# Kernel tuning notes

Measured on AMD Instinct MI355X. Metric: run time of the kernel, lower is better.

Reference implementation:

```python
import jax, jax.numpy as jnp
import numpy as np

EPS = 0.05  # blend weight of K_Rectify smoothing


def k_rectify(x_nbc, distance, idx, eps=EPS):
    """Distance-weighted neighbor smoothing.
    x_nbc: (N, B, C); distance, idx: (B, N, K). Returns (N, B, C)."""
    x_bnc = jnp.transpose(x_nbc, (1, 0, 2))                       # (B,N,C)
    B = x_bnc.shape[0]
    neigh = x_bnc[jnp.arange(B)[:, None, None], idx]              # (B,N,K,C) gather
    w = jax.nn.softmax(-distance, axis=-1)                        # closer -> larger weight
    smoothed = jnp.einsum('bnk,bnkc->bnc', w, neigh)              # (B,N,C)
    y = (1.0 - eps) * x_bnc + eps * smoothed
    return jnp.transpose(y, (1, 0, 2))


def monarch_linear(x, w1, w2, bias):
    """Monarch block-diagonal butterfly multiply on the last dim.
    w1: (k,q,p), w2: (l,s,r) with k*p == n, l*r == k*q."""
    shp = x.shape
    k, q, p = w1.shape
    l, s, r = w2.shape
    xb = x.reshape(-1, k, p)
    o1 = jnp.einsum('kqp,bkp->bkq', w1, xb)                       # (B*, k, q)
    o1 = o1.reshape(-1, r, l).transpose(0, 2, 1)                  # 'b (r l) -> b l r'
    o2 = jnp.einsum('lsr,blr->bls', w2, o1)                       # (B*, l, s)
    out = o2.transpose(0, 2, 1).reshape(-1, s * l) + bias         # 'b l s -> b (s l)'
    return out.reshape(*shp[:-1], s * l)


def setup_inputs() -> dict:
    key = jax.random.key(0)
    B, N, C, K, nblocks = 8, 8192, 256, 8, 8
    blk = C // nblocks
    ks = jax.random.split(key, 6)
    x = jax.random.normal(ks[0], (B, N, C), dtype=jnp.float32)
    distance = jax.random.uniform(ks[1], (B, N, K), dtype=jnp.float32)
    idx = jax.random.randint(ks[2], (B, N, K), 0, N)
    rf = jax.random.normal(ks[3], (B, N, C), dtype=jnp.float32)
    scale = 1.0 / np.sqrt(blk)
    w1 = jax.random.normal(ks[4], (nblocks, blk, blk), dtype=jnp.float32) * scale
    w2 = jax.random.normal(ks[5], (nblocks, blk, blk), dtype=jnp.float32) * scale
    bias = jnp.zeros((C,), dtype=jnp.float32)
    return {"x": x, "distance": distance, "idx": idx, "rf": rf,
            "w1": w1, "w2": w2, "bias": bias}


def reference(x, distance, idx, rf, w1, w2, bias):
    # _prepare_in: (B,N,C) -> (N,B,C)
    xs = jnp.transpose(x, (1, 0, 2))
    s1 = k_rectify(xs, distance, idx)            # smooth_in
    t = monarch_linear(s1, w1, w2, bias)         # Monarch block-diag matmul
    s2 = k_rectify(t, distance, idx)             # smooth_out
    return jnp.transpose(s2, (1, 0, 2)) + rf     # _out_transform residual
```

## Files before the change

### kernel.cpp

```cpp
#include <hip/hip_runtime.h>

#define NPTS 8192
#define CH   256
#define KNB  8
#define NROWS 65536
#define ROWS_PER_BLK 32
#define ROWS_PER_IT  4
#define FT_STRIDE 36

#define NBLK_CONV 8192
#define NBLK_S1   (NROWS / ROWS_PER_BLK)
#define NBLK_S2   (NROWS / 16)

typedef unsigned short ushort_t;
typedef float  f32x4  __attribute__((ext_vector_type(4)));

__device__ __forceinline__ int xcd_swz(int h, int cpx) {
    return (h & 7) * cpx + (h >> 3);
}

__device__ __forceinline__ ushort_t f32_to_bf16(float f) {
    unsigned int b = __float_as_uint(f);
    b += 0x7FFFu + ((b >> 16) & 1u);
    return (ushort_t)(b >> 16);
}
__device__ __forceinline__ float bf16_to_f32(ushort_t u) {
    return __uint_as_float(((unsigned int)u) << 16);
}
__device__ __forceinline__ unsigned int pack_bf16(float lo, float hi) {
    return (unsigned int)f32_to_bf16(lo) | ((unsigned int)f32_to_bf16(hi) << 16);
}

__global__ __launch_bounds__(256) void pm_conv(
    const f32x4* __restrict__ x, uint4* __restrict__ xb)
{
    const int l = xcd_swz(blockIdx.x, NBLK_CONV / 8);
    const size_t i = (size_t)l * 256 + threadIdx.x;
    const f32x4 a = __builtin_nontemporal_load(&x[2 * i]);
    const f32x4 c = __builtin_nontemporal_load(&x[2 * i + 1]);
    uint4 o;
    o.x = pack_bf16(a.x, a.y);
    o.y = pack_bf16(a.z, a.w);
    o.z = pack_bf16(c.x, c.y);
    o.w = pack_bf16(c.z, c.w);
    xb[i] = o;
}

__global__ __launch_bounds__(256) void pm_stage1(
    const ushort_t* __restrict__ xb, const float* __restrict__ dist,
    const int* __restrict__ idx, const float* __restrict__ w1,
    const float* __restrict__ w2, const float* __restrict__ bias,
    ushort_t* __restrict__ t)
{
    const int c = threadIdx.x;

    __shared__ float s1[ROWS_PER_IT][CH];
    __shared__ float fT[ROWS_PER_IT][8 * FT_STRIDE];

    float4 w1r[8], w2r[8];
    {
        const float4* w1p = (const float4*)(w1 + c * 32);
        const float4* w2p = (const float4*)(w2 + ((c & 7) * 32 + (c >> 3)) * 32);
#pragma unroll
        for (int i = 0; i < 8; ++i) { w1r[i] = w1p[i]; w2r[i] = w2p[i]; }
    }
    const float bb = bias[c];
    const int l2   = c & 7;
    const int kb   = c >> 5;
    const int ftw  = l2 * FT_STRIDE + (c >> 3);

    const int rr   = __builtin_amdgcn_readfirstlane(threadIdx.x >> 6);
    const int lane = threadIdx.x & 63;

    const int lb       = xcd_swz(blockIdx.x, NBLK_S1 / 8);
    const int row_base = lb * ROWS_PER_BLK;
    const int b = row_base >> 13;
    const ushort4* x4 = (const ushort4*)(xb + (size_t)b * NPTS * CH);

    for (int it = 0; it < ROWS_PER_BLK / ROWS_PER_IT; ++it) {
        const int row  = row_base + it * ROWS_PER_IT + rr;
        const int rloc = row & (NPTS - 1);

        float d[KNB]; int nb[KNB];
#pragma unroll
        for (int k = 0; k < KNB; ++k) {
            d[k]  = dist[(size_t)row * KNB + k];
            nb[k] = idx[(size_t)row * KNB + k];
        }

        const ushort4 c0 = x4[(size_t)rloc * 64 + lane];
        ushort4 g[KNB];
#pragma unroll
        for (int k = 0; k < KNB; ++k) g[k] = x4[(size_t)nb[k] * 64 + lane];

        float mn = d[0];
#pragma unroll
        for (int k = 1; k < KNB; ++k) mn = fminf(mn, d[k]);
        float e[KNB]; float sum = 0.f;
#pragma unroll
        for (int k = 0; k < KNB; ++k) { e[k] = __expf(mn - d[k]); sum += e[k]; }
        const float inv = 0.05f / sum;

        float4 acc;
        acc.x = 0.95f * bf16_to_f32(c0.x);
        acc.y = 0.95f * bf16_to_f32(c0.y);
        acc.z = 0.95f * bf16_to_f32(c0.z);
        acc.w = 0.95f * bf16_to_f32(c0.w);
#pragma unroll
        for (int k = 0; k < KNB; ++k) {
            const float w = e[k] * inv;
            acc.x += w * bf16_to_f32(g[k].x);
            acc.y += w * bf16_to_f32(g[k].y);
            acc.z += w * bf16_to_f32(g[k].z);
            acc.w += w * bf16_to_f32(g[k].w);
        }
        ((float4*)&s1[rr][0])[lane] = acc;
        __syncthreads();

#pragma unroll
        for (int r2 = 0; r2 < ROWS_PER_IT; ++r2) {
            const float4* sb = (const float4*)(&s1[r2][kb * 32]);
            float a = 0.f;
#pragma unroll
            for (int p4 = 0; p4 < 8; ++p4) {
                const float4 s = sb[p4];
                a += w1r[p4].x * s.x + w1r[p4].y * s.y
                   + w1r[p4].z * s.z + w1r[p4].w * s.w;
            }
            fT[r2][ftw] = a;
        }
        __syncthreads();

#pragma unroll
        for (int r2 = 0; r2 < ROWS_PER_IT; ++r2) {
            const float4* fp = (const float4*)(&fT[r2][l2 * FT_STRIDE]);
            float a = bb;
#pragma unroll
            for (int r4 = 0; r4 < 8; ++r4) {
                const float4 f = fp[r4];
                a += w2r[r4].x * f.x + w2r[r4].y * f.y
                   + w2r[r4].z * f.z + w2r[r4].w * f.w;
            }
            __builtin_nontemporal_store(
                f32_to_bf16(a),
                &t[(size_t)(row_base + it * ROWS_PER_IT + r2) * CH + c]);
        }
        __syncthreads();
    }
}

__global__ __launch_bounds__(256) void pm_stage2(
    const ushort_t* __restrict__ t, const float* __restrict__ dist,
    const int* __restrict__ idx, const float* __restrict__ rf,
    float* __restrict__ out)
{
    const int w     = __builtin_amdgcn_readfirstlane(threadIdx.x >> 6);
    const int lane  = threadIdx.x & 63;
    const int lb    = xcd_swz(blockIdx.x, NBLK_S2 / 8);
    const int wrow0 = lb * 16 + w * 4;
    const int b     = wrow0 >> 13;
    const ushort4* tb = (const ushort4*)(t + (size_t)b * NPTS * CH);

    int   nb[4][KNB];
    float d [4][KNB];
#pragma unroll
    for (int r = 0; r < 4; ++r)
#pragma unroll
        for (int k = 0; k < KNB; ++k) {
            nb[r][k] = idx[(size_t)(wrow0 + r) * KNB + k];
            d [r][k] = dist[(size_t)(wrow0 + r) * KNB + k];
        }

    ushort4 c0[4], g[4][KNB];
    f32x4   rv[4];
#pragma unroll
    for (int r = 0; r < 4; ++r) {
        const int rloc = (wrow0 + r) & (NPTS - 1);
        c0[r] = tb[(size_t)rloc * 64 + lane];
        rv[r] = __builtin_nontemporal_load(
                    &((const f32x4*)rf)[(size_t)(wrow0 + r) * 64 + lane]);
#pragma unroll
        for (int k = 0; k < KNB; ++k) g[r][k] = tb[(size_t)nb[r][k] * 64 + lane];
    }

#pragma unroll
    for (int r = 0; r < 4; ++r) {
        float mn = d[r][0];
#pragma unroll
        for (int k = 1; k < KNB; ++k) mn = fminf(mn, d[r][k]);
        float e[KNB]; float sum = 0.f;
#pragma unroll
        for (int k = 0; k < KNB; ++k) { e[k] = __expf(mn - d[r][k]); sum += e[k]; }
        const float inv = 0.05f / sum;

        f32x4 acc;
        acc.x = 0.95f * bf16_to_f32(c0[r].x) + rv[r].x;
        acc.y = 0.95f * bf16_to_f32(c0[r].y) + rv[r].y;
        acc.z = 0.95f * bf16_to_f32(c0[r].z) + rv[r].z;
        acc.w = 0.95f * bf16_to_f32(c0[r].w) + rv[r].w;
#pragma unroll
        for (int k = 0; k < KNB; ++k) {
            const float wk = e[k] * inv;
            acc.x += wk * bf16_to_f32(g[r][k].x);
            acc.y += wk * bf16_to_f32(g[r][k].y);
            acc.z += wk * bf16_to_f32(g[r][k].z);
            acc.w += wk * bf16_to_f32(g[r][k].w);
        }
        __builtin_nontemporal_store(
            acc, &((f32x4*)out)[(size_t)(wrow0 + r) * 64 + lane]);
    }
}

extern "C" void kernel_launch(void* const* d_in, const int* in_sizes, int n_in,
                              void* d_out, int out_size, void* d_ws, size_t ws_size,
                              hipStream_t stream) {
    const float* x    = (const float*)d_in[0];
    const float* dist = (const float*)d_in[1];
    const int*   idx  = (const int*)d_in[2];
    const float* rf   = (const float*)d_in[3];
    const float* w1   = (const float*)d_in[4];
    const float* w2   = (const float*)d_in[5];
    const float* bias = (const float*)d_in[6];
    float* out = (float*)d_out;

    ushort_t* t  = (ushort_t*)d_ws;
    ushort_t* xb = (ushort_t*)((char*)d_ws + (size_t)NROWS * CH * 2);

    pm_conv  <<<NBLK_CONV, 256, 0, stream>>>((const f32x4*)x, (uint4*)xb);
    pm_stage1<<<NBLK_S1,   256, 0, stream>>>(xb, dist, idx, w1, w2, bias, t);
    pm_stage2<<<NBLK_S2,   256, 0, stream>>>(t, dist, idx, rf, out);
}
```

Baseline: 270.1 us.

## Software-pipeline neighbor gathers in stage1 and scalarize index loads

Stage1 now prefetches the next iteration's distances, indices and neighbor gathers while the Monarch matmul for the current rows runs, and drops the trailing barrier per iteration. Barriers become a manual lgkmcnt wait plus s_barrier, so outstanding global loads are not drained at each sync. Index and distance loads are vectorized and neighbor indices are made wave-uniform via readfirstlane, so gather addresses become scalar. Launch bounds ask for 4 blocks per CU, which may limit registers, and the extra prefetched values raise register pressure.

```diff
diff --git a/kernel.cpp b/kernel.cpp
--- a/kernel.cpp
+++ b/kernel.cpp
@@ -6,6 +6,7 @@
 #define NROWS 65536
 #define ROWS_PER_BLK 32
 #define ROWS_PER_IT  4
+#define NIT (ROWS_PER_BLK / ROWS_PER_IT)
 #define FT_STRIDE 36
 
 #define NBLK_CONV 8192
@@ -14,6 +15,11 @@
 
 typedef unsigned short ushort_t;
 typedef float  f32x4  __attribute__((ext_vector_type(4)));
+
+#define BARRIER_LDS() do { \
+    asm volatile("s_waitcnt lgkmcnt(0)" ::: "memory"); \
+    __builtin_amdgcn_s_barrier(); \
+} while (0)
 
 __device__ __forceinline__ int xcd_swz(int h, int cpx) {
     return (h & 7) * cpx + (h >> 3);
@@ -46,7 +52,7 @@
     xb[i] = o;
 }
 
-__global__ __launch_bounds__(256) void pm_stage1(
+__global__ __launch_bounds__(256, 4) void pm_stage1(
     const ushort_t* __restrict__ xb, const float* __restrict__ dist,
     const int* __restrict__ idx, const float* __restrict__ w1,
     const float* __restrict__ w2, const float* __restrict__ bias,
@@ -75,30 +81,51 @@
     const int lb       = xcd_swz(blockIdx.x, NBLK_S1 / 8);
     const int row_base = lb * ROWS_PER_BLK;
     const int b = row_base >> 13;
-    const ushort4* x4 = (const ushort4*)(xb + (size_t)b * NPTS * CH);
-
-    for (int it = 0; it < ROWS_PER_BLK / ROWS_PER_IT; ++it) {
-        const int row  = row_base + it * ROWS_PER_IT + rr;
-        const int rloc = row & (NPTS - 1);
-
-        float d[KNB]; int nb[KNB];
-#pragma unroll
-        for (int k = 0; k < KNB; ++k) {
-            d[k]  = dist[(size_t)row * KNB + k];
-            nb[k] = idx[(size_t)row * KNB + k];
-        }
-
-        const ushort4 c0 = x4[(size_t)rloc * 64 + lane];
-        ushort4 g[KNB];
-#pragma unroll
-        for (int k = 0; k < KNB; ++k) g[k] = x4[(size_t)nb[k] * 64 + lane];
-
-        float mn = d[0];
-#pragma unroll
-        for (int k = 1; k < KNB; ++k) mn = fminf(mn, d[k]);
+    const char* xbase  = (const char*)(xb + (size_t)b * NPTS * CH);
+    const int laneoff  = lane * 8;
+
+    float dcur[KNB]; int nbs[KNB];
+    {
+        const int row = row_base + rr;
+        const float4 d0 = *(const float4*)(dist + (size_t)row * KNB);
+        const float4 d1 = *(const float4*)(dist + (size_t)row * KNB + 4);
+        const int4   i0 = *(const int4*)(idx + (size_t)row * KNB);
+        const int4   i1 = *(const int4*)(idx + (size_t)row * KNB + 4);
+        dcur[0]=d0.x; dcur[1]=d0.y; dcur[2]=d0.z; dcur[3]=d0.w;
+        dcur[4]=d1.x; dcur[5]=d1.y; dcur[6]=d1.z; dcur[7]=d1.w;
+        nbs[0]=__builtin_amdgcn_readfirstlane(i0.x);
+        nbs[1]=__builtin_amdgcn_readfirstlane(i0.y);
+        nbs[2]=__builtin_amdgcn_readfirstlane(i0.z);
+        nbs[3]=__builtin_amdgcn_readfirstlane(i0.w);
+        nbs[4]=__builtin_amdgcn_readfirstlane(i1.x);
+        nbs[5]=__builtin_amdgcn_readfirstlane(i1.y);
+        nbs[6]=__builtin_amdgcn_readfirstlane(i1.z);
+        nbs[7]=__builtin_amdgcn_readfirstlane(i1.w);
+    }
+    ushort4 c0, g[KNB];
+    {
+        const int rloc = (row_base + rr) & (NPTS - 1);
+        c0 = *(const ushort4*)(xbase + ((size_t)rloc << 9) + laneoff);
+#pragma unroll
+        for (int k = 0; k < KNB; ++k)
+            g[k] = *(const ushort4*)(xbase + ((size_t)(unsigned)nbs[k] << 9) + laneoff);
+    }
+
+    for (int it = 0; it < NIT; ++it) {
+        const bool more = (it + 1 < NIT);
+        const int rown  = row_base + (more ? it + 1 : it) * ROWS_PER_IT + rr;
+
+        const float4 dn0 = *(const float4*)(dist + (size_t)rown * KNB);
+        const float4 dn1 = *(const float4*)(dist + (size_t)rown * KNB + 4);
+        const int4   in0 = *(const int4*)(idx + (size_t)rown * KNB);
+        const int4   in1 = *(const int4*)(idx + (size_t)rown * KNB + 4);
+
+        float mn = dcur[0];
+#pragma unroll
+        for (int k = 1; k < KNB; ++k) mn = fminf(mn, dcur[k]);
         float e[KNB]; float sum = 0.f;
 #pragma unroll
-        for (int k = 0; k < KNB; ++k) { e[k] = __expf(mn - d[k]); sum += e[k]; }
+        for (int k = 0; k < KNB; ++k) { e[k] = __expf(mn - dcur[k]); sum += e[k]; }
         const float inv = 0.05f / sum;
 
         float4 acc;
@@ -115,7 +142,8 @@
             acc.w += w * bf16_to_f32(g[k].w);
         }
         ((float4*)&s1[rr][0])[lane] = acc;
-        __syncthreads();
+
+        BARRIER_LDS();
 
 #pragma unroll
         for (int r2 = 0; r2 < ROWS_PER_IT; ++r2) {
@@ -129,7 +157,26 @@
             }
             fT[r2][ftw] = a;
         }
-        __syncthreads();
+
+        if (more) {
+            dcur[0]=dn0.x; dcur[1]=dn0.y; dcur[2]=dn0.z; dcur[3]=dn0.w;
+            dcur[4]=dn1.x; dcur[5]=dn1.y; dcur[6]=dn1.z; dcur[7]=dn1.w;
+            nbs[0]=__builtin_amdgcn_readfirstlane(in0.x);
+            nbs[1]=__builtin_amdgcn_readfirstlane(in0.y);
+            nbs[2]=__builtin_amdgcn_readfirstlane(in0.z);
+            nbs[3]=__builtin_amdgcn_readfirstlane(in0.w);
+            nbs[4]=__builtin_amdgcn_readfirstlane(in1.x);
+            nbs[5]=__builtin_amdgcn_readfirstlane(in1.y);
+            nbs[6]=__builtin_amdgcn_readfirstlane(in1.z);
+            nbs[7]=__builtin_amdgcn_readfirstlane(in1.w);
+            const int rloc = rown & (NPTS - 1);
+            c0 = *(const ushort4*)(xbase + ((size_t)rloc << 9) + laneoff);
+#pragma unroll
+            for (int k = 0; k < KNB; ++k)
+                g[k] = *(const ushort4*)(xbase + ((size_t)(unsigned)nbs[k] << 9) + laneoff);
+        }
+
+        BARRIER_LDS();
 
 #pragma unroll
         for (int r2 = 0; r2 < ROWS_PER_IT; ++r2) {
@@ -145,11 +192,10 @@
                 f32_to_bf16(a),
                 &t[(size_t)(row_base + it * ROWS_PER_IT + r2) * CH + c]);
         }
-        __syncthreads();
-    }
-}
-
-__global__ __launch_bounds__(256) void pm_stage2(
+    }
+}
+
+__global__ __launch_bounds__(256, 4) void pm_stage2(
     const ushort_t* __restrict__ t, const float* __restrict__ dist,
     const int* __restrict__ idx, const float* __restrict__ rf,
     float* __restrict__ out)
@@ -159,28 +205,41 @@
     const int lb    = xcd_swz(blockIdx.x, NBLK_S2 / 8);
     const int wrow0 = lb * 16 + w * 4;
     const int b     = wrow0 >> 13;
-    const ushort4* tb = (const ushort4*)(t + (size_t)b * NPTS * CH);
-
-    int   nb[4][KNB];
+    const char* tbase = (const char*)(t + (size_t)b * NPTS * CH);
+    const int laneoff = lane * 8;
+
+    int   nbs[4][KNB];
     float d [4][KNB];
 #pragma unroll
-    for (int r = 0; r < 4; ++r)
-#pragma unroll
-        for (int k = 0; k < KNB; ++k) {
-            nb[r][k] = idx[(size_t)(wrow0 + r) * KNB + k];
-            d [r][k] = dist[(size_t)(wrow0 + r) * KNB + k];
-        }
+    for (int r = 0; r < 4; ++r) {
+        const int row = wrow0 + r;
+        const float4 d0 = *(const float4*)(dist + (size_t)row * KNB);
+        const float4 d1 = *(const float4*)(dist + (size_t)row * KNB + 4);
+        const int4   i0 = *(const int4*)(idx + (size_t)row * KNB);
+        const int4   i1 = *(const int4*)(idx + (size_t)row * KNB + 4);
+        d[r][0]=d0.x; d[r][1]=d0.y; d[r][2]=d0.z; d[r][3]=d0.w;
+        d[r][4]=d1.x; d[r][5]=d1.y; d[r][6]=d1.z; d[r][7]=d1.w;
+        nbs[r][0]=__builtin_amdgcn_readfirstlane(i0.x);
+        nbs[r][1]=__builtin_amdgcn_readfirstlane(i0.y);
+        nbs[r][2]=__builtin_amdgcn_readfirstlane(i0.z);
+        nbs[r][3]=__builtin_amdgcn_readfirstlane(i0.w);
+        nbs[r][4]=__builtin_amdgcn_readfirstlane(i1.x);
+        nbs[r][5]=__builtin_amdgcn_readfirstlane(i1.y);
+        nbs[r][6]=__builtin_amdgcn_readfirstlane(i1.z);
+        nbs[r][7]=__builtin_amdgcn_readfirstlane(i1.w);
+    }
 
     ushort4 c0[4], g[4][KNB];
     f32x4   rv[4];
 #pragma unroll
     for (int r = 0; r < 4; ++r) {
         const int rloc = (wrow0 + r) & (NPTS - 1);
-        c0[r] = tb[(size_t)rloc * 64 + lane];
+        c0[r] = *(const ushort4*)(tbase + ((size_t)rloc << 9) + laneoff);
         rv[r] = __builtin_nontemporal_load(
                     &((const f32x4*)rf)[(size_t)(wrow0 + r) * 64 + lane]);
 #pragma unroll
-        for (int k = 0; k < KNB; ++k) g[r][k] = tb[(size_t)nb[r][k] * 64 + lane];
+        for (int k = 0; k < KNB; ++k)
+            g[r][k] = *(const ushort4*)(tbase + ((size_t)(unsigned)nbs[r][k] << 9) + laneoff);
     }
 
 #pragma unroll
```

Result: no change. 267.0 us (-1.1%).
